# Optimization experiments

Measured on AMD Instinct MI355X. Metric: run time of the kernel, lower is better.

Reference implementation:

```python
import jax, jax.numpy as jnp
import numpy as np

E = 8           # num_local_experts
H = 1024        # hidden_size
F = 1024        # moe_ffn_hidden_size (per-half; fc1 out = 2*F due to GLU)
T = 16384       # total dispatched tokens
GLU_LINEAR_OFFSET = 1.0


def setup_inputs() -> dict:
    key = jax.random.key(0)
    ks = jax.random.split(key, 7)
    s1 = 1.0 / np.sqrt(H)
    s2 = 1.0 / np.sqrt(F)
    return {
        "hidden_states": jax.random.normal(ks[0], (T, H), jnp.float32),
        "tokens_per_expert": jnp.full((E,), T // E, dtype=jnp.int64),
        "probs": jax.random.uniform(ks[1], (T,), jnp.float32),
        # expert params; torch Linear W is [out,in], stored here as [in,out] (same math)
        "W1": jax.random.uniform(ks[2], (E, H, 2 * F), jnp.float32, -s1, s1),
        "b1": jax.random.uniform(ks[3], (E, 2 * F), jnp.float32, -s1, s1),
        "W2": jax.random.uniform(ks[4], (E, F, H), jnp.float32, -s2, s2),
        "b2": jax.random.uniform(ks[5], (E, H), jnp.float32, -s2, s2),
    }


def reference(hidden_states, tokens_per_expert, probs, W1, b1, W2, b2):
    # Tokens arrive grouped contiguously by expert with equal counts (as in
    # setup_inputs), so the split/loop/cat in the torch module is exactly a
    # reshape + grouped (batched) GEMM over the expert axis.
    e = W1.shape[0]
    t, h = hidden_states.shape
    x = hidden_states.reshape(e, t // e, h)            # [E, Tpe, H]
    p = probs.reshape(e, t // e)                       # [E, Tpe]
    # fc1 (gated)
    y = jnp.einsum('eth,ehf->etf', x, W1) + b1[:, None, :]  # [E, Tpe, 2F]
    gate, lin = jnp.split(y, 2, axis=-1)
    a = jax.nn.silu(gate) * (lin + GLU_LINEAR_OFFSET)       # [E, Tpe, F]
    a = a * p[..., None]                                    # per-token scale
    # fc2
    out = jnp.einsum('etf,efh->eth', a, W2) + b2[:, None, :]
    return out.reshape(t, h)
```

## Files before the change

kernel.cpp:

```cpp
#include <hip/hip_runtime.h>
#include <hip/hip_bf16.h>
#include <stdint.h>

#define T_TOK 16384
#define H_DIM 1024
#define F_DIM 1024
#define E_NUM 8
#define TPE   2048

typedef unsigned short u16;
typedef __attribute__((ext_vector_type(8))) short bf16x8;
typedef __attribute__((ext_vector_type(4))) float f32x4;
typedef __attribute__((ext_vector_type(8))) u16 u16x8;

__device__ __forceinline__ u16 f2bf(float x) {
  unsigned int u = __float_as_uint(x);
  u = (u + 0x7fffu + ((u >> 16) & 1u)) >> 16;
  return (u16)u;
}

#define GLD16(gp, lp)                                                          \
  __builtin_amdgcn_global_load_lds(                                            \
      (const __attribute__((address_space(1))) void*)(gp),                     \
      (__attribute__((address_space(3))) void*)(lp), 16, 0, 0)

__global__ __launch_bounds__(256) void cvt_f32_bf16(
    const float* __restrict__ src, u16* __restrict__ dst, int n8) {
  int stride = gridDim.x * blockDim.x;
  for (int i = blockIdx.x * blockDim.x + threadIdx.x; i < n8; i += stride) {
    const float4* s = (const float4*)(src + (size_t)i * 8);
    float4 a = s[0], b = s[1];
    u16x8 o;
    o[0] = f2bf(a.x); o[1] = f2bf(a.y); o[2] = f2bf(a.z); o[3] = f2bf(a.w);
    o[4] = f2bf(b.x); o[5] = f2bf(b.y); o[6] = f2bf(b.z); o[7] = f2bf(b.w);
    *(u16x8*)(dst + (size_t)i * 8) = o;
  }
}

__global__ __launch_bounds__(256) void transpose_cvt(
    const float* __restrict__ src, u16* __restrict__ dst, int R, int C) {
  __shared__ float tile[64][65];
  int nCt = C >> 6, nRt = R >> 6;
  int per = nCt * nRt;
  int b = blockIdx.x;
  int e = b / per;
  int r2 = b - e * per;
  int rt = r2 / nCt, ct = r2 - rt * nCt;
  const float* s = src + (size_t)e * R * C + (size_t)(rt << 6) * C + (ct << 6);
  int t = threadIdx.x;
  int lr = t >> 4, lc = (t & 15) << 2;
#pragma unroll
  for (int i = 0; i < 4; i++) {
    float4 v = *(const float4*)(s + (size_t)(lr + i * 16) * C + lc);
    tile[lr + i * 16][lc + 0] = v.x;
    tile[lr + i * 16][lc + 1] = v.y;
    tile[lr + i * 16][lc + 2] = v.z;
    tile[lr + i * 16][lc + 3] = v.w;
  }
  __syncthreads();
  u16* d = dst + (size_t)e * C * R + (size_t)(ct << 6) * R + (rt << 6);
  int orow = t >> 2, ok = (t & 3) << 4;
  u16x8 o0, o1;
#pragma unroll
  for (int i = 0; i < 8; i++) o0[i] = f2bf(tile[ok + i][orow]);
#pragma unroll
  for (int i = 0; i < 8; i++) o1[i] = f2bf(tile[ok + 8 + i][orow]);
  *(u16x8*)(d + (size_t)orow * R + ok) = o0;
  *(u16x8*)(d + (size_t)orow * R + ok + 8) = o1;
}


#define DSA(b, mi)                                                             \
  _Pragma("unroll") for (int m2_ = 0; m2_ < 2; ++m2_)                          \
  _Pragma("unroll") for (int ks_ = 0; ks_ < 2; ++ks_)                          \
      aF[m2_][ks_] = *(const bf16x8*)(sm + (b) * 32768 + aRowBase +            \
                                      ((mi) * 2 + m2_) * 2048 + koff[ks_]);

#define DSB(b)                                                                 \
  _Pragma("unroll") for (int n_ = 0; n_ < 4; ++n_)                             \
  _Pragma("unroll") for (int ks_ = 0; ks_ < 2; ++ks_)                          \
      bF[n_][ks_] = *(const bf16x8*)(sm + 65536 + (b) * 32768 + bRowBase +     \
                                     n_ * 2048 + koff[ks_]);

#define MFMA16(mi)                                                             \
  _Pragma("unroll") for (int n_ = 0; n_ < 4; ++n_)                             \
  _Pragma("unroll") for (int m2_ = 0; m2_ < 2; ++m2_)                          \
  _Pragma("unroll") for (int ks_ = 0; ks_ < 2; ++ks_)                          \
      acc[(mi) * 2 + m2_][n_] = __builtin_amdgcn_mfma_f32_16x16x32_bf16(       \
          aF[m2_][ks_], bF[n_][ks_], acc[(mi) * 2 + m2_][n_], 0, 0, 0);

#define PF_A(db, q, d) GLD16(aP[q] + (d), sm + (db) * 32768 + (q) * 8192 + tid * 16)
#define PF_B(db, q, d) GLD16(bP[q] + (d), sm + 65536 + (db) * 32768 + (q) * 8192 + tid * 16)

#define PHASE(b, mi, PFC, WTC)                                                 \
  do {                                                                         \
    DSA(b, mi);                                                                \
    if ((mi) == 0) { DSB(b); }                                                 \
    PFC                                                                        \
    __builtin_amdgcn_s_setprio(1);                                             \
    MFMA16(mi);                                                                \
    __builtin_amdgcn_s_setprio(0);                                             \
    WTC                                                                        \
    __builtin_amdgcn_s_barrier();                                              \
  } while (0)

#define KLOOP_BODY                                                             \
  PF_B(0, 0, 0); PF_B(0, 1, 0); PF_B(0, 2, 0); PF_B(0, 3, 0);                  \
  PF_A(0, 0, 0); PF_A(0, 1, 0); PF_A(0, 2, 0); PF_A(0, 3, 0);                  \
  PF_B(1, 0, 64); PF_B(1, 1, 64); PF_B(1, 2, 64); PF_B(1, 3, 64);              \
  asm volatile("s_waitcnt vmcnt(4)" ::: "memory");                             \
  __builtin_amdgcn_s_barrier();                                                \
  for (int it = 0; it < 7; ++it) {                                             \
    PHASE(0, 0, PF_A(1, 0, 64); PF_A(1, 1, 64);, );                            \
    PHASE(0, 1, PF_A(1, 2, 64); PF_A(1, 3, 64);, );                            \
    PHASE(0, 2, PF_B(0, 0, 128); PF_B(0, 1, 128);, );                          \
    PHASE(0, 3, PF_B(0, 2, 128); PF_B(0, 3, 128);,                             \
          asm volatile("s_waitcnt vmcnt(4)" ::: "memory"););                   \
    PHASE(1, 0, PF_A(0, 0, 128); PF_A(0, 1, 128);, );                          \
    PHASE(1, 1, PF_A(0, 2, 128); PF_A(0, 3, 128);, );                          \
    PHASE(1, 2, PF_B(1, 0, 192); PF_B(1, 1, 192);, );                          \
    PHASE(1, 3, PF_B(1, 2, 192); PF_B(1, 3, 192);,                             \
          asm volatile("s_waitcnt vmcnt(4)" ::: "memory"););                   \
    _Pragma("unroll") for (int q_ = 0; q_ < 4; ++q_) {                         \
      aP[q_] += 128; bP[q_] += 128;                                            \
    }                                                                          \
  }                                                                            \
  PHASE(0, 0, PF_A(1, 0, 64); PF_A(1, 1, 64);, );                              \
  PHASE(0, 1, PF_A(1, 2, 64); PF_A(1, 3, 64);, );                              \
  PHASE(0, 2, , );                                                             \
  PHASE(0, 3, , asm volatile("s_waitcnt vmcnt(0)" ::: "memory"););             \
  PHASE(1, 0, , );                                                             \
  PHASE(1, 1, , );                                                             \
  PHASE(1, 2, , );                                                             \
  PHASE(1, 3, , );

__global__ __launch_bounds__(512, 2) void gemm1_8p(
    const u16* __restrict__ xbf, const u16* __restrict__ w1t,
    const float* __restrict__ b1, const float* __restrict__ probs,
    u16* __restrict__ abf) {
  extern __shared__ char sm[];
  const int tid = threadIdx.x;
  const int lane = tid & 63;
  const int wid = tid >> 6;
  const int wm = wid >> 2, wn = wid & 3;
  const int bid = blockIdx.x;
  const int e = bid & 7;
  const int inner = bid >> 3;
  const int mt = inner >> 3, ct = inner & 7;
  const int tokBase = e * TPE + mt * 256;
  const int c0 = ct * 128;
  const int lrow = lane & 15, lkhi = lane >> 4;

  const u16* aP[4]; const u16* bP[4];
#pragma unroll
  for (int q = 0; q < 4; ++q) {
    int lin = q * 8192 + tid * 16;
    int lg = lin ^ (((lin >> 7) & 7) << 4);
    int row = lg >> 7, kk = (lg & 127) >> 1;
    aP[q] = xbf + (size_t)(tokBase + row) * H_DIM + kk;
    int col = (((row >> 5) & 1) << 10) + c0 + ((row >> 6) << 5) + (row & 31);
    bP[q] = w1t + (size_t)(e * 2 * F_DIM + col) * H_DIM + kk;
  }
  const int aRowBase = (wm * 128 + lrow) * 128;
  const int bRowBase = (wn * 64 + lrow) * 128;
  int koff[2];
#pragma unroll
  for (int ks = 0; ks < 2; ++ks)
    koff[ks] = ((ks << 6) | (lkhi << 4)) ^ ((lane & 7) << 4);

  f32x4 acc[8][4];
#pragma unroll
  for (int i = 0; i < 8; ++i)
#pragma unroll
    for (int j = 0; j < 4; ++j) acc[i][j] = f32x4{0.f, 0.f, 0.f, 0.f};
  bf16x8 aF[2][2], bF[4][2];

  KLOOP_BODY

#pragma unroll
  for (int j = 0; j < 2; ++j) {
    int cf = c0 + wn * 32 + j * 16 + lrow;
    float gb = b1[e * 2 * F_DIM + cf];
    float lb = b1[e * 2 * F_DIM + F_DIM + cf];
#pragma unroll
    for (int i = 0; i < 8; ++i) {
      int trow = tokBase + wm * 128 + i * 16 + lkhi * 4;
#pragma unroll
      for (int r = 0; r < 4; ++r) {
        float g = acc[i][j][r] + gb;
        float l = acc[i][j + 2][r] + lb + 1.0f;
        float p = probs[trow + r];
        float sig = 1.0f / (1.0f + __expf(-g));
        abf[(size_t)(trow + r) * F_DIM + cf] = f2bf(g * sig * l * p);
      }
    }
  }
}

__global__ __launch_bounds__(512, 2) void gemm2_8p(
    const u16* __restrict__ abf, const u16* __restrict__ w2t,
    const float* __restrict__ b2, float* __restrict__ out) {
  extern __shared__ char sm[];
  const int tid = threadIdx.x;
  const int lane = tid & 63;
  const int wid = tid >> 6;
  const int wm = wid >> 2, wn = wid & 3;
  const int bid = blockIdx.x;
  const int e = bid & 7;
  const int inner = bid >> 3;
  const int mt = inner >> 2, nt = inner & 3;
  const int tokBase = e * TPE + mt * 256;
  const int h0 = nt * 256;
  const int lrow = lane & 15, lkhi = lane >> 4;

  const u16* aP[4]; const u16* bP[4];
#pragma unroll
  for (int q = 0; q < 4; ++q) {
    int lin = q * 8192 + tid * 16;
    int lg = lin ^ (((lin >> 7) & 7) << 4);
    int row = lg >> 7, kk = (lg & 127) >> 1;
    aP[q] = abf + (size_t)(tokBase + row) * F_DIM + kk;
    bP[q] = w2t + (size_t)(e * H_DIM + h0 + row) * F_DIM + kk;
  }
  const int aRowBase = (wm * 128 + lrow) * 128;
  const int bRowBase = (wn * 64 + lrow) * 128;
  int koff[2];
#pragma unroll
  for (int ks = 0; ks < 2; ++ks)
    koff[ks] = ((ks << 6) | (lkhi << 4)) ^ ((lane & 7) << 4);

  f32x4 acc[8][4];
#pragma unroll
  for (int i = 0; i < 8; ++i)
#pragma unroll
    for (int j = 0; j < 4; ++j) acc[i][j] = f32x4{0.f, 0.f, 0.f, 0.f};
  bf16x8 aF[2][2], bF[4][2];

  KLOOP_BODY

#pragma unroll
  for (int j = 0; j < 4; ++j) {
    int h = h0 + wn * 64 + j * 16 + lrow;
    float bb = b2[e * H_DIM + h];
#pragma unroll
    for (int i = 0; i < 8; ++i) {
      int trow = tokBase + wm * 128 + i * 16 + lkhi * 4;
#pragma unroll
      for (int r = 0; r < 4; ++r)
        out[(size_t)(trow + r) * H_DIM + h] = acc[i][j][r] + bb;
    }
  }
}

extern "C" void kernel_launch(void* const* d_in, const int* in_sizes, int n_in,
                              void* d_out, int out_size, void* d_ws,
                              size_t ws_size, hipStream_t stream) {
  const float* x     = (const float*)d_in[0];
  const float* probs = (const float*)d_in[2];
  const float* W1    = (const float*)d_in[3];
  const float* b1    = (const float*)d_in[4];
  const float* W2    = (const float*)d_in[5];
  const float* b2    = (const float*)d_in[6];
  float* out = (float*)d_out;

  if (ws_size < 117440512u) return;
  char* ws = (char*)d_ws;
  u16* xbf = (u16*)(ws);
  u16* w1t = (u16*)(ws + 33554432);
  u16* w2t = (u16*)(ws + 67108864);
  u16* abf = (u16*)(ws + 83886080);

  (void)hipFuncSetAttribute(reinterpret_cast<const void*>(gemm1_8p),
                            hipFuncAttributeMaxDynamicSharedMemorySize, 131072);
  (void)hipFuncSetAttribute(reinterpret_cast<const void*>(gemm2_8p),
                            hipFuncAttributeMaxDynamicSharedMemorySize, 131072);

  cvt_f32_bf16<<<2048, 256, 0, stream>>>(x, xbf, (T_TOK * H_DIM) / 8);
  transpose_cvt<<<E_NUM * (2 * F_DIM / 64) * (H_DIM / 64), 256, 0, stream>>>(
      W1, w1t, H_DIM, 2 * F_DIM);
  transpose_cvt<<<E_NUM * (H_DIM / 64) * (F_DIM / 64), 256, 0, stream>>>(
      W2, w2t, F_DIM, H_DIM);
  gemm1_8p<<<E_NUM * 8 * 8, 512, 131072, stream>>>(xbf, w1t, b1, probs, abf);
  gemm2_8p<<<E_NUM * 8 * 4, 512, 131072, stream>>>(abf, w2t, b2, out);
}
```

Baseline: 157.7 us.

## Split each K=64 stage by k-slice to shrink fragment registers and regroup B prefetch

Each 64-wide K stage is now split into two k-slices, and each slice into two M-halves. A phase loads 4 A fragments, plus 4 B fragments for the first half, and issues 16 MFMAs. Fragment registers drop from 12 to 8 bf16x8 vectors, and the four B prefetches for the next stage are issued together in the last phase instead of across two phases. The aim is lower register pressure at two waves per SIMD and a different interleave of LDS reads and global loads, at the cost of LDS reloads per k-slice and a changed point at which B data becomes available.

After: 158.9 us. About the same (+0.8%).

```diff
diff --git a/kernel.cpp b/kernel.cpp
--- a/kernel.cpp
+++ b/kernel.cpp
@@ -70,35 +70,34 @@
 }
 
 
-#define DSA(b, mi)                                                             \
-  _Pragma("unroll") for (int m2_ = 0; m2_ < 2; ++m2_)                          \
-  _Pragma("unroll") for (int ks_ = 0; ks_ < 2; ++ks_)                          \
-      aF[m2_][ks_] = *(const bf16x8*)(sm + (b) * 32768 + aRowBase +            \
-                                      ((mi) * 2 + m2_) * 2048 + koff[ks_]);
-
-#define DSB(b)                                                                 \
+#define DSA4(b, h, ks)                                                         \
+  _Pragma("unroll") for (int m_ = 0; m_ < 4; ++m_)                             \
+      aF[m_] = *(const bf16x8*)(sm + (b) * 32768 + aRowBase +                  \
+                                ((h) * 4 + m_) * 2048 + koff[ks]);
+
+#define DSB4(b, ks)                                                            \
   _Pragma("unroll") for (int n_ = 0; n_ < 4; ++n_)                             \
-  _Pragma("unroll") for (int ks_ = 0; ks_ < 2; ++ks_)                          \
-      bF[n_][ks_] = *(const bf16x8*)(sm + 65536 + (b) * 32768 + bRowBase +     \
-                                     n_ * 2048 + koff[ks_]);
-
-#define MFMA16(mi)                                                             \
+      bF[n_] = *(const bf16x8*)(sm + 65536 + (b) * 32768 + bRowBase +          \
+                                n_ * 2048 + koff[ks]);
+
+#define MFMAP(h)                                                               \
   _Pragma("unroll") for (int n_ = 0; n_ < 4; ++n_)                             \
-  _Pragma("unroll") for (int m2_ = 0; m2_ < 2; ++m2_)                          \
-  _Pragma("unroll") for (int ks_ = 0; ks_ < 2; ++ks_)                          \
-      acc[(mi) * 2 + m2_][n_] = __builtin_amdgcn_mfma_f32_16x16x32_bf16(       \
-          aF[m2_][ks_], bF[n_][ks_], acc[(mi) * 2 + m2_][n_], 0, 0, 0);
+  _Pragma("unroll") for (int m_ = 0; m_ < 4; ++m_)                             \
+      acc[(h) * 4 + m_][n_] = __builtin_amdgcn_mfma_f32_16x16x32_bf16(         \
+          aF[m_], bF[n_], acc[(h) * 4 + m_][n_], 0, 0, 0);
 
 #define PF_A(db, q, d) GLD16(aP[q] + (d), sm + (db) * 32768 + (q) * 8192 + tid * 16)
 #define PF_B(db, q, d) GLD16(bP[q] + (d), sm + 65536 + (db) * 32768 + (q) * 8192 + tid * 16)
 
-#define PHASE(b, mi, PFC, WTC)                                                 \
+#define VMW(N) asm volatile("s_waitcnt vmcnt(" #N ")" ::: "memory");
+
+#define PHASEK(b, ks, h, PFC, WTC)                                             \
   do {                                                                         \
-    DSA(b, mi);                                                                \
-    if ((mi) == 0) { DSB(b); }                                                 \
+    DSA4(b, h, ks);                                                            \
+    if ((h) == 0) { DSB4(b, ks); }                                             \
     PFC                                                                        \
     __builtin_amdgcn_s_setprio(1);                                             \
-    MFMA16(mi);                                                                \
+    MFMAP(h);                                                                  \
     __builtin_amdgcn_s_setprio(0);                                             \
     WTC                                                                        \
     __builtin_amdgcn_s_barrier();                                              \
@@ -108,31 +107,34 @@
   PF_B(0, 0, 0); PF_B(0, 1, 0); PF_B(0, 2, 0); PF_B(0, 3, 0);                  \
   PF_A(0, 0, 0); PF_A(0, 1, 0); PF_A(0, 2, 0); PF_A(0, 3, 0);                  \
   PF_B(1, 0, 64); PF_B(1, 1, 64); PF_B(1, 2, 64); PF_B(1, 3, 64);              \
-  asm volatile("s_waitcnt vmcnt(4)" ::: "memory");                             \
+  VMW(4)                                                                       \
   __builtin_amdgcn_s_barrier();                                                \
   for (int it = 0; it < 7; ++it) {                                             \
-    PHASE(0, 0, PF_A(1, 0, 64); PF_A(1, 1, 64);, );                            \
-    PHASE(0, 1, PF_A(1, 2, 64); PF_A(1, 3, 64);, );                            \
-    PHASE(0, 2, PF_B(0, 0, 128); PF_B(0, 1, 128);, );                          \
-    PHASE(0, 3, PF_B(0, 2, 128); PF_B(0, 3, 128);,                             \
-          asm volatile("s_waitcnt vmcnt(4)" ::: "memory"););                   \
-    PHASE(1, 0, PF_A(0, 0, 128); PF_A(0, 1, 128);, );                          \
-    PHASE(1, 1, PF_A(0, 2, 128); PF_A(0, 3, 128);, );                          \
-    PHASE(1, 2, PF_B(1, 0, 192); PF_B(1, 1, 192);, );                          \
-    PHASE(1, 3, PF_B(1, 2, 192); PF_B(1, 3, 192);,                             \
-          asm volatile("s_waitcnt vmcnt(4)" ::: "memory"););                   \
+    PHASEK(0, 0, 0, PF_A(1, 0, 64); PF_A(1, 1, 64);, );                        \
+    PHASEK(0, 0, 1, PF_A(1, 2, 64); PF_A(1, 3, 64);, );                        \
+    PHASEK(0, 1, 0, , );                                                       \
+    PHASEK(0, 1, 1,                                                            \
+           PF_B(0, 0, 128); PF_B(0, 1, 128); PF_B(0, 2, 128);                  \
+           PF_B(0, 3, 128);, VMW(4));                                          \
+    PHASEK(1, 0, 0, PF_A(0, 0, 128); PF_A(0, 1, 128);, );                      \
+    PHASEK(1, 0, 1, PF_A(0, 2, 128); PF_A(0, 3, 128);, );                      \
+    PHASEK(1, 1, 0, , );                                                       \
+    PHASEK(1, 1, 1,                                                            \
+           PF_B(1, 0, 192); PF_B(1, 1, 192); PF_B(1, 2, 192);                  \
+           PF_B(1, 3, 192);, VMW(4));                                          \
     _Pragma("unroll") for (int q_ = 0; q_ < 4; ++q_) {                         \
       aP[q_] += 128; bP[q_] += 128;                                            \
     }                                                                          \
   }                                                                            \
-  PHASE(0, 0, PF_A(1, 0, 64); PF_A(1, 1, 64);, );                              \
-  PHASE(0, 1, PF_A(1, 2, 64); PF_A(1, 3, 64);, );                              \
-  PHASE(0, 2, , );                                                             \
-  PHASE(0, 3, , asm volatile("s_waitcnt vmcnt(0)" ::: "memory"););             \
-  PHASE(1, 0, , );                                                             \
-  PHASE(1, 1, , );                                                             \
-  PHASE(1, 2, , );                                                             \
-  PHASE(1, 3, , );
+                   \
+  PHASEK(0, 0, 0, PF_A(1, 0, 64); PF_A(1, 1, 64);, );                          \
+  PHASEK(0, 0, 1, PF_A(1, 2, 64); PF_A(1, 3, 64);, );                          \
+  PHASEK(0, 1, 0, , );                                                         \
+  PHASEK(0, 1, 1, , VMW(0));                                                   \
+  PHASEK(1, 0, 0, , );                                                         \
+  PHASEK(1, 0, 1, , );                                                         \
+  PHASEK(1, 1, 0, , );                                                         \
+  PHASEK(1, 1, 1, , );
 
 __global__ __launch_bounds__(512, 2) void gemm1_8p(
     const u16* __restrict__ xbf, const u16* __restrict__ w1t,
@@ -173,7 +175,7 @@
   for (int i = 0; i < 8; ++i)
 #pragma unroll
     for (int j = 0; j < 4; ++j) acc[i][j] = f32x4{0.f, 0.f, 0.f, 0.f};
-  bf16x8 aF[2][2], bF[4][2];
+  bf16x8 aF[4], bF[4];
 
   KLOOP_BODY
 
@@ -234,7 +236,7 @@
   for (int i = 0; i < 8; ++i)
 #pragma unroll
     for (int j = 0; j < 4; ++j) acc[i][j] = f32x4{0.f, 0.f, 0.f, 0.f};
-  bf16x8 aF[2][2], bF[4][2];
+  bf16x8 aF[4], bF[4];
 
   KLOOP_BODY
 
```
